# Optimization experiments

Hardware: AMD Instinct MI355X
Metric: run time of the kernel (lower is better)

Reference implementation:

```python
import jax, jax.numpy as jnp
import numpy as np

N_NODES = 100000
N_EDGES = 1600000
IN_CH, HID_CH, OUT_CH = 128, 64, 64


def setup_inputs() -> dict:
    key = jax.random.key(0)
    ks = jax.random.split(key, 9)
    def glorot(k, shape):
        lim = jnp.sqrt(6.0 / (shape[0] + shape[1]))
        return jax.random.uniform(k, shape, jnp.float32, -lim, lim)
    return {
        "x": jax.random.normal(ks[0], (N_NODES, IN_CH), jnp.float32),
        "edge_src": jax.random.randint(ks[1], (N_EDGES,), 0, N_NODES, jnp.int32),
        "edge_dst": jax.random.randint(ks[2], (N_EDGES,), 0, N_NODES, jnp.int32),
        "W1": glorot(ks[3], (IN_CH, HID_CH)),
        "b1": jnp.zeros((HID_CH,), jnp.float32),
        "W2": glorot(ks[4], (HID_CH, HID_CH)),
        "b2": jnp.zeros((HID_CH,), jnp.float32),
        "W3": glorot(ks[5], (HID_CH, OUT_CH)),
        "b3": jnp.zeros((OUT_CH,), jnp.float32),
    }


def _gcn_layer(h, W, b, edge_src, edge_dst):
    # GCNConv(normalize=False): transform then sum-aggregate over incoming edges
    hw = h @ W                                   # [N, d_out]
    msg = hw[edge_src]                           # [E, d_out] gather
    agg = jax.ops.segment_sum(msg, edge_dst, num_segments=N_NODES)  # scatter-add
    return agg + b


def reference(x, edge_src, edge_dst, W1, b1, W2, b2, W3, b3):
    # layer 1 + relu (dropout is identity at inference)
    h = jax.nn.relu(_gcn_layer(x, W1, b1, edge_src, edge_dst))
    # layer 2 + relu
    h = jax.nn.relu(_gcn_layer(h, W2, b2, edge_src, edge_dst))
    # final layer, no activation
    return _gcn_layer(h, W3, b3, edge_src, edge_dst)
```

## Files before the change

kernel.cpp:

```cpp
#include <hip/hip_runtime.h>

#define CH 64
#define BNODES 128
#define NB_MAX 1024
#define CUR_PAD 16
#define SCAT_CHUNK 8192
#define SCAT_THREADS 1024
#define BSLACK 1024
#define HIST_BLOCKS 256

typedef unsigned short ushort_t;
typedef unsigned int uint_t;
typedef short short8_t __attribute__((ext_vector_type(8)));
typedef float float4_t __attribute__((ext_vector_type(4)));

static __device__ __forceinline__ ushort_t f2bf(float x) {
    uint_t u = __float_as_uint(x);
    u = (u + 0x7FFFu + ((u >> 16) & 1u)) >> 16;
    return (ushort_t)u;
}
static __device__ __forceinline__ float bflo(uint_t u) {
    return __uint_as_float(u << 16);
}
static __device__ __forceinline__ float bfhi(uint_t u) {
    return __uint_as_float(u & 0xFFFF0000u);
}

__global__ __launch_bounds__(256) void prep_kernel(
    const float* __restrict__ W1, const float* __restrict__ W2, const float* __restrict__ W3,
    ushort_t* __restrict__ Wt1, ushort_t* __restrict__ Wt2, ushort_t* __restrict__ Wt3,
    int* __restrict__ bcnt, int NB)
{
    const int b = blockIdx.x;
    if (b == 3) {
        for (int i = threadIdx.x; i < NB; i += 256) bcnt[i] = 0;
        return;
    }
    const float* W = (b == 0) ? W1 : (b == 1) ? W2 : W3;
    ushort_t* Wt   = (b == 0) ? Wt1 : (b == 1) ? Wt2 : Wt3;
    const int K    = (b == 0) ? 128 : 64;
    for (int i = threadIdx.x; i < K * CH; i += 256) {
        int n = i / K, k = i % K;
        Wt[i] = f2bf(W[(size_t)k * CH + n]);
    }
}

template<int K, typename T>
static __device__ __forceinline__ void gemm_body(
    const T* __restrict__ h, const ushort_t* __restrict__ Wt,
    ushort_t* __restrict__ outb, int n, ushort_t* Hs, int blockRow)
{
    constexpr int LDH = K + 8;
    constexpr int C8  = K / 8;
    constexpr int KC  = K / 32;

    const int t    = threadIdx.x;
    const int lane = t & 63;
    const int wv   = t >> 6;
    const int l15  = lane & 15;
    const int quad = lane >> 4;
    const int row0 = blockRow * 128;

    short8_t bfrag[4][KC];
    #pragma unroll
    for (int nt = 0; nt < 4; ++nt)
        #pragma unroll
        for (int kc = 0; kc < KC; ++kc)
            bfrag[nt][kc] = *(const short8_t*)(Wt + (size_t)(nt * 16 + l15) * K + kc * 32 + quad * 8);

    for (int idx = t; idx < 128 * C8; idx += 256) {
        int r  = idx / C8;
        int c8 = idx % C8;
        int rg = row0 + r;
        short8_t v = (short8_t)0;
        if (rg < n) {
            if constexpr (sizeof(T) == 4) {
                const float* p = (const float*)h + (size_t)rg * K + c8 * 8;
                float4 f0 = *(const float4*)p;
                float4 f1 = *(const float4*)(p + 4);
                v[0] = (short)f2bf(f0.x); v[1] = (short)f2bf(f0.y);
                v[2] = (short)f2bf(f0.z); v[3] = (short)f2bf(f0.w);
                v[4] = (short)f2bf(f1.x); v[5] = (short)f2bf(f1.y);
                v[6] = (short)f2bf(f1.z); v[7] = (short)f2bf(f1.w);
            } else {
                v = *(const short8_t*)((const ushort_t*)h + (size_t)rg * K + c8 * 8);
            }
        }
        *(short8_t*)&Hs[r * LDH + c8 * 8] = v;
    }
    __syncthreads();

    float4_t acc[2][4];
    #pragma unroll
    for (int mi = 0; mi < 2; ++mi)
        #pragma unroll
        for (int nt = 0; nt < 4; ++nt)
            acc[mi][nt] = (float4_t)0.f;

    #pragma unroll
    for (int kc = 0; kc < KC; ++kc) {
        short8_t a0 = *(const short8_t*)&Hs[(wv * 32 +      l15) * LDH + kc * 32 + quad * 8];
        short8_t a1 = *(const short8_t*)&Hs[(wv * 32 + 16 + l15) * LDH + kc * 32 + quad * 8];
        #pragma unroll
        for (int nt = 0; nt < 4; ++nt) {
            acc[0][nt] = __builtin_amdgcn_mfma_f32_16x16x32_bf16(a0, bfrag[nt][kc], acc[0][nt], 0, 0, 0);
            acc[1][nt] = __builtin_amdgcn_mfma_f32_16x16x32_bf16(a1, bfrag[nt][kc], acc[1][nt], 0, 0, 0);
        }
    }

    #pragma unroll
    for (int mi = 0; mi < 2; ++mi) {
        #pragma unroll
        for (int r = 0; r < 4; ++r) {
            int row = row0 + wv * 32 + mi * 16 + quad * 4 + r;
            if (row <= n) {
                #pragma unroll
                for (int nt = 0; nt < 4; ++nt)
                    outb[(size_t)row * CH + nt * 16 + l15] = f2bf(acc[mi][nt][r]);
            }
        }
    }
}

template<int K, typename T>
__global__ __launch_bounds__(256) void gemm_mfma(
    const T* __restrict__ h, const ushort_t* __restrict__ Wt,
    ushort_t* __restrict__ outb, int n)
{
    __shared__ ushort_t Hs[128 * (K + 8)];
    gemm_body<K, T>(h, Wt, outb, n, Hs, blockIdx.x);
}

__global__ __launch_bounds__(256) void gemm1_hist(
    const float* __restrict__ x, const ushort_t* __restrict__ Wt1,
    ushort_t* __restrict__ outb, int n,
    const int* __restrict__ dst, int* __restrict__ bcnt, int E, int NB, int gemmGrid)
{
    __shared__ ushort_t Hs[128 * 136];
    if (blockIdx.x >= gemmGrid) {
        int* h = (int*)Hs;
        const int t = threadIdx.x;
        for (int i = t; i < NB; i += 256) h[i] = 0;
        __syncthreads();
        for (int i = (blockIdx.x - gemmGrid) * 256 + t; i < E; i += HIST_BLOCKS * 256)
            atomicAdd(&h[dst[i] >> 7], 1);
        __syncthreads();
        for (int i = t; i < NB; i += 256) {
            int v = h[i];
            if (v) atomicAdd(&bcnt[i], v);
        }
        return;
    }
    gemm_body<128, float>(x, Wt1, outb, n, Hs, blockIdx.x);
}

__global__ __launch_bounds__(256) void bucket_scan(
    const int* __restrict__ bcnt, int* __restrict__ boff,
    int* __restrict__ cursor, int NB)
{
    __shared__ int tsum[256];
    int t = threadIdx.x;
    int base = t * 4;
    int c[4];
    #pragma unroll
    for (int j = 0; j < 4; ++j) {
        int i = base + j;
        c[j] = (i < NB) ? bcnt[i] : 0;
    }
    int local = c[0] + c[1] + c[2] + c[3];
    tsum[t] = local;
    __syncthreads();
    for (int off = 1; off < 256; off <<= 1) {
        int v = (t >= off) ? tsum[t - off] : 0;
        __syncthreads();
        tsum[t] += v;
        __syncthreads();
    }
    int p = tsum[t] - local;
    #pragma unroll
    for (int j = 0; j < 4; ++j) {
        int i = base + j;
        if (i < NB) { boff[i] = p; cursor[i * CUR_PAD] = p; }
        p += c[j];
    }
    if (t == 255) boff[NB] = tsum[255];
}

__global__ __launch_bounds__(SCAT_THREADS) void bucket_scatter_blk(
    const int* __restrict__ src, const int* __restrict__ dst,
    int* __restrict__ cursor, int* __restrict__ bucketed, int E, int NB)
{
    __shared__ int hist[NB_MAX];
    __shared__ int rbase[NB_MAX];
    __shared__ int lcur[NB_MAX];

    const int t = threadIdx.x;
    const int s = blockIdx.x * SCAT_CHUNK;
    const int e = min(s + SCAT_CHUNK, E);

    for (int i = t; i < NB; i += SCAT_THREADS) hist[i] = 0;
    __syncthreads();

    for (int i = s + t; i < e; i += SCAT_THREADS)
        atomicAdd(&hist[dst[i] >> 7], 1);
    __syncthreads();

    for (int i = t; i < NB; i += SCAT_THREADS) {
        int c = hist[i];
        rbase[i] = c ? atomicAdd(&cursor[i * CUR_PAD], c) : 0;
        lcur[i] = 0;
    }
    __syncthreads();

    for (int i = s + t; i < e; i += SCAT_THREADS) {
        int d = dst[i];
        int b = d >> 7;
        int p = atomicAdd(&lcur[b], 1);
        bucketed[rbase[b] + p] = ((d & 127) << 17) | src[i];
    }
}

__global__ __launch_bounds__(256) void node_sort(
    const int* __restrict__ bucketed, const int* __restrict__ boff,
    int* __restrict__ sorted_src, int2* __restrict__ seg, int N, int zrow)
{
    __shared__ int cnt[BNODES];
    __shared__ int sc[BNODES];
    __shared__ int cur[BNODES];
    const int bk = blockIdx.x;
    const int t  = threadIdx.x;
    const int s  = boff[bk];
    const int e  = boff[bk + 1];
    const int sbase = (s + bk * BSLACK + 7) & ~7;

    if (t < BNODES) cnt[t] = 0;
    __syncthreads();
    for (int i = s + t; i < e; i += 256)
        atomicAdd(&cnt[((unsigned)bucketed[i]) >> 17], 1);
    __syncthreads();

    int pc = 0;
    if (t < BNODES) { pc = (cnt[t] + 7) & ~7; sc[t] = pc; }
    __syncthreads();
    for (int o = 1; o < BNODES; o <<= 1) {
        int v = (t < BNODES && t >= o) ? sc[t - o] : 0;
        __syncthreads();
        if (t < BNODES) sc[t] += v;
        __syncthreads();
    }
    if (t < BNODES) {
        int pexcl = sc[t] - pc;
        cur[t] = pexcl;
        int node = bk * BNODES + t;
        if (node < N) seg[node] = make_int2(sbase + pexcl, pc);
        for (int k = cnt[t]; k < pc; ++k)
            sorted_src[sbase + pexcl + k] = zrow << 4;
    }
    __syncthreads();

    for (int i = s + t; i < e; i += 256) {
        int p = bucketed[i];
        int d = ((unsigned)p) >> 17;
        int pos = atomicAdd(&cur[d], 1);
        sorted_src[sbase + pos] = (p & 0x1FFFF) << 4;
    }
}

template<bool BF16_RELU_OUT>
__global__ __launch_bounds__(256) void aggregate_kernel(
    const ushort_t* __restrict__ hwb, const int* __restrict__ sorted_src,
    const int2* __restrict__ seg, const float* __restrict__ bias,
    ushort_t* __restrict__ outb, float* __restrict__ outf, int N)
{
    const int t    = threadIdx.x;
    const int lane = t & 63;
    const int node = blockIdx.x * 4 + (t >> 6);
    if (node >= N) return;

    int2 scv  = seg[node];
    int  base = __builtin_amdgcn_readfirstlane(scv.x);
    int  pc   = __builtin_amdgcn_readfirstlane(scv.y);

    const int g = lane >> 4;
    const int c = lane & 15;
    const uint2* hw2 = (const uint2*)hwb;
    const int*   sp  = sorted_src + base;

    float a0 = 0.f, a1 = 0.f, a2 = 0.f, a3 = 0.f;

    int u = 0;
    for (; u + 16 <= pc; u += 16) {
        int r0 = sp[u +      g];
        int r1 = sp[u +  4 + g];
        int r2 = sp[u +  8 + g];
        int r3 = sp[u + 12 + g];
        uint2 v0 = hw2[(size_t)(r0 + c)];
        uint2 v1 = hw2[(size_t)(r1 + c)];
        uint2 v2 = hw2[(size_t)(r2 + c)];
        uint2 v3 = hw2[(size_t)(r3 + c)];
        a0 += bflo(v0.x); a1 += bfhi(v0.x); a2 += bflo(v0.y); a3 += bfhi(v0.y);
        a0 += bflo(v1.x); a1 += bfhi(v1.x); a2 += bflo(v1.y); a3 += bfhi(v1.y);
        a0 += bflo(v2.x); a1 += bfhi(v2.x); a2 += bflo(v2.y); a3 += bfhi(v2.y);
        a0 += bflo(v3.x); a1 += bfhi(v3.x); a2 += bflo(v3.y); a3 += bfhi(v3.y);
    }
    if (u < pc) {
        int r0 = sp[u +     g];
        int r1 = sp[u + 4 + g];
        uint2 v0 = hw2[(size_t)(r0 + c)];
        uint2 v1 = hw2[(size_t)(r1 + c)];
        a0 += bflo(v0.x); a1 += bfhi(v0.x); a2 += bflo(v0.y); a3 += bfhi(v0.y);
        a0 += bflo(v1.x); a1 += bfhi(v1.x); a2 += bflo(v1.y); a3 += bfhi(v1.y);
    }

    a0 += __shfl_xor(a0, 16); a1 += __shfl_xor(a1, 16);
    a2 += __shfl_xor(a2, 16); a3 += __shfl_xor(a3, 16);
    a0 += __shfl_xor(a0, 32); a1 += __shfl_xor(a1, 32);
    a2 += __shfl_xor(a2, 32); a3 += __shfl_xor(a3, 32);

    float4 bv = *(const float4*)(bias + 4 * c);
    a0 += bv.x; a1 += bv.y; a2 += bv.z; a3 += bv.w;

    if (lane < 16) {
        if (BF16_RELU_OUT) {
            uint_t lo = (uint_t)f2bf(fmaxf(a0, 0.f)) | ((uint_t)f2bf(fmaxf(a1, 0.f)) << 16);
            uint_t hi = (uint_t)f2bf(fmaxf(a2, 0.f)) | ((uint_t)f2bf(fmaxf(a3, 0.f)) << 16);
            ((uint2*)outb)[(size_t)node * 16 + c] = make_uint2(lo, hi);
        } else {
            *(float4*)(outf + (size_t)node * CH + 4 * c) = make_float4(a0, a1, a2, a3);
        }
    }
}

extern "C" void kernel_launch(void* const* d_in, const int* in_sizes, int n_in,
                              void* d_out, int out_size, void* d_ws, size_t ws_size,
                              hipStream_t stream) {
    const float* x    = (const float*)d_in[0];
    const int*   esrc = (const int*)  d_in[1];
    const int*   edst = (const int*)  d_in[2];
    const float* W1   = (const float*)d_in[3];
    const float* b1   = (const float*)d_in[4];
    const float* W2   = (const float*)d_in[5];
    const float* b2   = (const float*)d_in[6];
    const float* W3   = (const float*)d_in[7];
    const float* b3   = (const float*)d_in[8];
    float* out = (float*)d_out;

    const int N  = in_sizes[0] / 128;
    const int E  = in_sizes[1];
    const int NB = (N + BNODES - 1) / BNODES;

    char* ws = (char*)d_ws;
    ushort_t* hwb   = (ushort_t*)ws; ws += (size_t)(N + 1) * CH * 2;
    ushort_t* hb    = (ushort_t*)ws; ws += (size_t)N * CH * 2;
    int* bucketed   = (int*)ws;      ws += (size_t)E * 4;
    ws = (char*)(((uintptr_t)ws + 15) & ~(uintptr_t)15);
    int* sorted_src = (int*)ws;      ws += ((size_t)E + (size_t)NB * BSLACK + 64) * 4;
    int2* seg       = (int2*)ws;     ws += (size_t)N * 8;
    int* bcnt       = (int*)ws;      ws += (size_t)NB * 4;
    int* boff       = (int*)ws;      ws += (size_t)(NB + 1) * 4;
    ws = (char*)(((uintptr_t)ws + 63) & ~(uintptr_t)63);
    int* cursor     = (int*)ws;      ws += (size_t)NB * CUR_PAD * 4;
    ws = (char*)(((uintptr_t)ws + 15) & ~(uintptr_t)15);
    ushort_t* Wt1   = (ushort_t*)ws; ws += (size_t)CH * 128 * 2;
    ushort_t* Wt2   = (ushort_t*)ws; ws += (size_t)CH * 64 * 2;
    ushort_t* Wt3   = (ushort_t*)ws; ws += (size_t)CH * 64 * 2;

    dim3 blk(256);
    int gemmGrid = (N + 1 + 127) / 128;
    int aggGrid  = (N + 3) / 4;
    int scatGrid = (E + SCAT_CHUNK - 1) / SCAT_CHUNK;

    prep_kernel<<<4, blk, 0, stream>>>(W1, W2, W3, Wt1, Wt2, Wt3, bcnt, NB);

    gemm1_hist<<<gemmGrid + HIST_BLOCKS, blk, 0, stream>>>(
        x, Wt1, hwb, N, edst, bcnt, E, NB, gemmGrid);

    bucket_scan<<<1, blk, 0, stream>>>(bcnt, boff, cursor, NB);
    bucket_scatter_blk<<<scatGrid, dim3(SCAT_THREADS), 0, stream>>>(esrc, edst, cursor, bucketed, E, NB);
    node_sort<<<NB, blk, 0, stream>>>(bucketed, boff, sorted_src, seg, N, N );

    aggregate_kernel<true><<<aggGrid, blk, 0, stream>>>(hwb, sorted_src, seg, b1, hb, nullptr, N);
    gemm_mfma<64, ushort_t><<<gemmGrid, blk, 0, stream>>>(hb, Wt2, hwb, N);
    aggregate_kernel<true><<<aggGrid, blk, 0, stream>>>(hwb, sorted_src, seg, b2, hb, nullptr, N);
    gemm_mfma<64, ushort_t><<<gemmGrid, blk, 0, stream>>>(hb, Wt3, hwb, N);
    aggregate_kernel<false><<<aggGrid, blk, 0, stream>>>(hwb, sorted_src, seg, b3, nullptr, out, N);
}
```

Baseline: 309.8 us.

## Aggregate four nodes per wavefront with software-prefetched neighbor indices

Each wavefront in the aggregation kernel now handles four destination nodes at once and interleaves their gathers. Neighbor indices for the next 8-edge chunk are loaded before the current chunk is accumulated, so index loads overlap with the feature gathers. This aims to raise memory-level parallelism and hide gather latency. In exchange the four nodes run in lockstep up to the largest degree among them, which wastes lanes when degrees differ, and register pressure rises.

```diff
diff --git a/kernel.cpp b/kernel.cpp
--- a/kernel.cpp
+++ b/kernel.cpp
@@ -274,59 +274,93 @@
 {
     const int t    = threadIdx.x;
     const int lane = t & 63;
-    const int node = blockIdx.x * 4 + (t >> 6);
-    if (node >= N) return;
-
-    int2 scv  = seg[node];
-    int  base = __builtin_amdgcn_readfirstlane(scv.x);
-    int  pc   = __builtin_amdgcn_readfirstlane(scv.y);
-
-    const int g = lane >> 4;
-    const int c = lane & 15;
+    const int wv   = t >> 6;
+    const int g    = lane >> 4;
+    const int c    = lane & 15;
+    const int nb   = (blockIdx.x * 4 + wv) * 4;
+
     const uint2* hw2 = (const uint2*)hwb;
-    const int*   sp  = sorted_src + base;
-
-    float a0 = 0.f, a1 = 0.f, a2 = 0.f, a3 = 0.f;
-
-    int u = 0;
-    for (; u + 16 <= pc; u += 16) {
-        int r0 = sp[u +      g];
-        int r1 = sp[u +  4 + g];
-        int r2 = sp[u +  8 + g];
-        int r3 = sp[u + 12 + g];
-        uint2 v0 = hw2[(size_t)(r0 + c)];
-        uint2 v1 = hw2[(size_t)(r1 + c)];
-        uint2 v2 = hw2[(size_t)(r2 + c)];
-        uint2 v3 = hw2[(size_t)(r3 + c)];
-        a0 += bflo(v0.x); a1 += bfhi(v0.x); a2 += bflo(v0.y); a3 += bfhi(v0.y);
-        a0 += bflo(v1.x); a1 += bfhi(v1.x); a2 += bflo(v1.y); a3 += bfhi(v1.y);
-        a0 += bflo(v2.x); a1 += bfhi(v2.x); a2 += bflo(v2.y); a3 += bfhi(v2.y);
-        a0 += bflo(v3.x); a1 += bfhi(v3.x); a2 += bflo(v3.y); a3 += bfhi(v3.y);
-    }
-    if (u < pc) {
-        int r0 = sp[u +     g];
-        int r1 = sp[u + 4 + g];
-        uint2 v0 = hw2[(size_t)(r0 + c)];
-        uint2 v1 = hw2[(size_t)(r1 + c)];
-        a0 += bflo(v0.x); a1 += bfhi(v0.x); a2 += bflo(v0.y); a3 += bfhi(v0.y);
-        a0 += bflo(v1.x); a1 += bfhi(v1.x); a2 += bflo(v1.y); a3 += bfhi(v1.y);
-    }
-
-    a0 += __shfl_xor(a0, 16); a1 += __shfl_xor(a1, 16);
-    a2 += __shfl_xor(a2, 16); a3 += __shfl_xor(a3, 16);
-    a0 += __shfl_xor(a0, 32); a1 += __shfl_xor(a1, 32);
-    a2 += __shfl_xor(a2, 32); a3 += __shfl_xor(a3, 32);
+
+    int base[4], pcnt[4];
+    #pragma unroll
+    for (int i = 0; i < 4; ++i) {
+        int node = nb + i;
+        if (node < N) {
+            int2 s = seg[node];
+            base[i] = __builtin_amdgcn_readfirstlane(s.x);
+            pcnt[i] = __builtin_amdgcn_readfirstlane(s.y);
+        } else {
+            base[i] = 0; pcnt[i] = 0;
+        }
+    }
+
+    float a0[4], a1[4], a2[4], a3[4];
+    #pragma unroll
+    for (int i = 0; i < 4; ++i) { a0[i] = a1[i] = a2[i] = a3[i] = 0.f; }
+
+    int maxpc = max(max(pcnt[0], pcnt[1]), max(pcnt[2], pcnt[3]));
+
+    int r0[4], r1[4];
+    #pragma unroll
+    for (int i = 0; i < 4; ++i) {
+        if (0 < pcnt[i]) {
+            const int* sp = sorted_src + base[i];
+            r0[i] = sp[g];
+            r1[i] = sp[4 + g];
+        }
+    }
+
+    for (int u = 0; u < maxpc; u += 8) {
+        uint2 v0[4], v1[4];
+        #pragma unroll
+        for (int i = 0; i < 4; ++i) {
+            if (u < pcnt[i]) {
+                v0[i] = hw2[(size_t)(r0[i] + c)];
+                v1[i] = hw2[(size_t)(r1[i] + c)];
+            }
+        }
+        int n0[4], n1[4];
+        #pragma unroll
+        for (int i = 0; i < 4; ++i) {
+            if (u + 8 < pcnt[i]) {
+                const int* sp = sorted_src + base[i] + u + 8;
+                n0[i] = sp[g];
+                n1[i] = sp[4 + g];
+            }
+        }
+        #pragma unroll
+        for (int i = 0; i < 4; ++i) {
+            if (u < pcnt[i]) {
+                a0[i] += bflo(v0[i].x); a1[i] += bfhi(v0[i].x);
+                a2[i] += bflo(v0[i].y); a3[i] += bfhi(v0[i].y);
+                a0[i] += bflo(v1[i].x); a1[i] += bfhi(v1[i].x);
+                a2[i] += bflo(v1[i].y); a3[i] += bfhi(v1[i].y);
+            }
+        }
+        #pragma unroll
+        for (int i = 0; i < 4; ++i) { r0[i] = n0[i]; r1[i] = n1[i]; }
+    }
 
     float4 bv = *(const float4*)(bias + 4 * c);
-    a0 += bv.x; a1 += bv.y; a2 += bv.z; a3 += bv.w;
-
-    if (lane < 16) {
-        if (BF16_RELU_OUT) {
-            uint_t lo = (uint_t)f2bf(fmaxf(a0, 0.f)) | ((uint_t)f2bf(fmaxf(a1, 0.f)) << 16);
-            uint_t hi = (uint_t)f2bf(fmaxf(a2, 0.f)) | ((uint_t)f2bf(fmaxf(a3, 0.f)) << 16);
-            ((uint2*)outb)[(size_t)node * 16 + c] = make_uint2(lo, hi);
-        } else {
-            *(float4*)(outf + (size_t)node * CH + 4 * c) = make_float4(a0, a1, a2, a3);
+
+    #pragma unroll
+    for (int i = 0; i < 4; ++i) {
+        int node = nb + i;
+        if (node >= N) continue;
+        float s0 = a0[i], s1 = a1[i], s2 = a2[i], s3 = a3[i];
+        s0 += __shfl_xor(s0, 16); s1 += __shfl_xor(s1, 16);
+        s2 += __shfl_xor(s2, 16); s3 += __shfl_xor(s3, 16);
+        s0 += __shfl_xor(s0, 32); s1 += __shfl_xor(s1, 32);
+        s2 += __shfl_xor(s2, 32); s3 += __shfl_xor(s3, 32);
+        s0 += bv.x; s1 += bv.y; s2 += bv.z; s3 += bv.w;
+        if (lane < 16) {
+            if (BF16_RELU_OUT) {
+                uint_t lo = (uint_t)f2bf(fmaxf(s0, 0.f)) | ((uint_t)f2bf(fmaxf(s1, 0.f)) << 16);
+                uint_t hi = (uint_t)f2bf(fmaxf(s2, 0.f)) | ((uint_t)f2bf(fmaxf(s3, 0.f)) << 16);
+                ((uint2*)outb)[(size_t)node * 16 + c] = make_uint2(lo, hi);
+            } else {
+                *(float4*)(outf + (size_t)node * CH + 4 * c) = make_float4(s0, s1, s2, s3);
+            }
         }
     }
 }
@@ -367,7 +401,7 @@
 
     dim3 blk(256);
     int gemmGrid = (N + 1 + 127) / 128;
-    int aggGrid  = (N + 3) / 4;
+    int aggGrid  = (N + 15) / 16;
     int scatGrid = (E + SCAT_CHUNK - 1) / SCAT_CHUNK;
 
     prep_kernel<<<4, blk, 0, stream>>>(W1, W2, W3, Wt1, Wt2, Wt3, bcnt, NB);
```

After: 340.2 us. +9.8%, slower.
